# Kernel tuning notes

Hardware: AMD Instinct MI355X
Metric: run time of the kernel (lower is better)

## Reference

```python
import jax, jax.numpy as jnp
import numpy as np


def setup_inputs() -> dict:
    key = jax.random.key(0)
    ks = jax.random.split(key, 5)
    B, T, D, U, O = 128, 512, 512, 1024, 512
    x = jax.random.normal(ks[0], (B, T, D), dtype=jnp.float32)
    h0 = jnp.zeros((B, U), dtype=jnp.float32)
    c0 = jnp.zeros((B, U), dtype=jnp.float32)
    # Keras LSTMCell params: kernel [D,4U], recurrent_kernel [U,4U], bias [4U]; gate order i,f,g,o
    kernel = jax.random.normal(ks[1], (D, 4 * U), dtype=jnp.float32) * (1.0 / np.sqrt(D))
    rec_kernel = jax.random.normal(ks[2], (U, 4 * U), dtype=jnp.float32) * (1.0 / np.sqrt(U))
    bias = jnp.zeros((4 * U,), dtype=jnp.float32)
    Wd = jax.random.normal(ks[3], (U, O), dtype=jnp.float32) * (1.0 / np.sqrt(U))
    bd = jnp.zeros((O,), dtype=jnp.float32)
    return {"x": x, "h0": h0, "c0": c0, "kernel": kernel, "rec_kernel": rec_kernel,
            "bias": bias, "Wd": Wd, "bd": bd}


def _lstm_decode(x, h0, c0, kernel, rec_kernel, bias, Wd, bd):
    U = h0.shape[-1]
    # Precompute input contribution for all timesteps in one big GEMM: [B,T,4U]
    xz = jnp.einsum("btd,dg->btg", x, kernel) + bias

    def step(carry, xz_t):
        h, c = carry
        z = xz_t + h @ rec_kernel                     # [B,4U]
        i, f, g, o = jnp.split(z, 4, axis=-1)         # Keras gate order i,f,g,o
        i = jax.nn.sigmoid(i)
        f = jax.nn.sigmoid(f)
        o = jax.nn.sigmoid(o)
        c = f * c + i * jnp.tanh(g)
        h = o * jnp.tanh(c)
        return (h, c), h

    (_, _), hs = jax.lax.scan(step, (h0, c0), jnp.swapaxes(xz, 0, 1))  # hs: [T,B,U]
    hs = jnp.swapaxes(hs, 0, 1)                       # [B,T,U]
    # Per-step dense projection (output_layer of BasicDecoder)
    return jnp.einsum("btu,uo->bto", hs, Wd) + bd


def reference(x, h0, c0, kernel, rec_kernel, bias, Wd, bd):
    return _lstm_decode(x, h0, c0, kernel, rec_kernel, bias, Wd, bd)
```

## Files before the change

kernel.cpp:

```cpp
#include <hip/hip_runtime.h>
#include <hip/hip_bf16.h>

#define B_   128
#define T_   512
#define D_   512
#define U_   1024
#define O_   512
#define K_   1536
#define G4U_ 4096
#define NBLK 256
#define HPITCH 1032

typedef __attribute__((ext_vector_type(8))) short short8;
typedef __attribute__((ext_vector_type(4))) float f32x4;
typedef __attribute__((ext_vector_type(4))) int int4v;

__device__ __align__(16) unsigned short g_xbf[(size_t)B_ * T_ * D_];
__device__ __align__(16) unsigned short g_Wt[(size_t)G4U_ * K_];
__device__ __align__(16) unsigned short g_Wdt[(size_t)O_ * U_];
__device__ __align__(16) unsigned short g_hall[(size_t)(T_ + 1) * B_ * U_];
__device__ unsigned int g_flag[NBLK * 32];

__device__ __forceinline__ unsigned short f2b(float f) {
  unsigned u = __float_as_uint(f);
  u += 0x7fffu + ((u >> 16) & 1u);
  return (unsigned short)(u >> 16);
}

__global__ void prep_kernel(const float* __restrict__ x, const float* __restrict__ h0,
                            const float* __restrict__ kern, const float* __restrict__ rkern,
                            const float* __restrict__ Wd) {
  size_t tid = (size_t)blockIdx.x * blockDim.x + threadIdx.x;
  size_t np  = (size_t)gridDim.x * blockDim.x;
  if (tid < NBLK * 32) g_flag[tid] = 0u;

  const size_t nx8 = (size_t)B_ * T_ * D_ / 8;
  const float4* xv = (const float4*)x;
  for (size_t i = tid; i < nx8; i += np) {
    float4 v0 = xv[2 * i], v1 = xv[2 * i + 1];
    unsigned short tmp[8];
    tmp[0] = f2b(v0.x); tmp[1] = f2b(v0.y); tmp[2] = f2b(v0.z); tmp[3] = f2b(v0.w);
    tmp[4] = f2b(v1.x); tmp[5] = f2b(v1.y); tmp[6] = f2b(v1.z); tmp[7] = f2b(v1.w);
    *(int4*)&g_xbf[i * 8] = *(const int4*)tmp;
  }

  const size_t nw = (size_t)G4U_ * (K_ / 8);
  for (size_t i = tid; i < nw; i += np) {
    size_t cg = i / (K_ / 8);
    int kb = (int)(i % (K_ / 8)) * 8;
    int c = (int)(cg >> 6), g = (int)((cg >> 4) & 3), j = (int)(cg & 15);
    int n = g * 1024 + (c << 4) + j;
    unsigned short tmp[8];
#pragma unroll
    for (int q = 0; q < 8; ++q) {
      int k = kb + q;
      float v = (k < 512) ? kern[(size_t)k * G4U_ + n] : rkern[(size_t)(k - 512) * G4U_ + n];
      tmp[q] = f2b(v);
    }
    *(int4*)&g_Wt[cg * K_ + kb] = *(const int4*)tmp;
  }

  const size_t nd = (size_t)O_ * (U_ / 8);
  for (size_t i = tid; i < nd; i += np) {
    int o  = (int)(i >> 7);
    int ub = (int)(i & 127) * 8;
    unsigned short tmp[8];
#pragma unroll
    for (int q = 0; q < 8; ++q) tmp[q] = f2b(Wd[(size_t)(ub + q) * O_ + o]);
    *(int4*)&g_Wdt[(size_t)o * U_ + ub] = *(const int4*)tmp;
  }

  const size_t nh = (size_t)B_ * U_;
  for (size_t i = tid; i < nh; i += np) g_hall[i] = f2b(h0[i]);
}

__global__ __launch_bounds__(256, 1) void lstm_kernel(const float* __restrict__ c0,
                                                      const float* __restrict__ bias,
                                                      const float* __restrict__ bd,
                                                      float* __restrict__ out) {
  const int b    = blockIdx.x;
  const int tid  = threadIdx.x;
  const int wq   = tid >> 6;
  const int lane = tid & 63;
  const int rg   = lane >> 4;
  const int fr   = lane & 15;

  const int xcd = b & 7, idx = b >> 3;
  const int mg  = xcd >> 1;
  const int sl  = idx * 2 + (xcd & 1);
  const int lb  = mg * 64 + sl;
  const int m0  = mg * 32;
  const int ug  = sl;
  const int u0  = ug * 16;

  __shared__ __align__(16) unsigned short Ast[32 * HPITCH];
  __shared__ f32x4 zpo[4][32][17];
  __shared__ float po[4][16][20];

  short8 wzx[4][4], wzh[8][4];
#pragma unroll
  for (int kt = 0; kt < 4; ++kt)
#pragma unroll
    for (int g = 0; g < 4; ++g)
      wzx[kt][g] = *(const short8*)&g_Wt[(size_t)(ug * 64 + g * 16 + fr) * K_ +
                                         wq * 128 + kt * 32 + rg * 8];
#pragma unroll
  for (int kt = 0; kt < 8; ++kt)
#pragma unroll
    for (int g = 0; g < 4; ++g)
      wzh[kt][g] = *(const short8*)&g_Wt[(size_t)(ug * 64 + g * 16 + fr) * K_ +
                                         512 + wq * 256 + kt * 32 + rg * 8];

  const int oc0 = (ug >> 1) * 16;
  const int orh = (ug & 1) * 16;
  short8 wd[8];
#pragma unroll
  for (int kt = 0; kt < 8; ++kt)
    wd[kt] = *(const short8*)&g_Wdt[(size_t)(oc0 + fr) * U_ + wq * 256 + kt * 32 + rg * 8];

  const int erow = tid >> 3;
  const int euu  = (tid & 7) * 2;
  float cv[2];
  f32x4 bv[2];
#pragma unroll
  for (int j = 0; j < 2; ++j) {
    cv[j] = c0[(size_t)(m0 + erow) * U_ + u0 + euu + j];
    f32x4 tv;
#pragma unroll
    for (int g = 0; g < 4; ++g) tv[g] = bias[g * 1024 + u0 + euu + j];
    bv[j] = tv;
  }

  const int orow = tid >> 4, ocl = tid & 15;
  const float bd_v = bd[oc0 + ocl];

  const int xcol = wq * 128 + rg * 8;
  const unsigned short* ahp0 = &Ast[(size_t)fr * HPITCH + wq * 256 + rg * 8];
  const unsigned short* ahp1 = ahp0 + 16 * HPITCH;
  const unsigned short* aop  = &Ast[(size_t)(orh + fr) * HPITCH + wq * 256 + rg * 8];

  const int srow = lane >> 5;
  const int sseg = lane & 31;

  short8 axf0[4], axf1[4];
  {
    const unsigned short* x0 = &g_xbf[((size_t)(m0 + fr) * T_ + 0) * D_ + xcol];
    const unsigned short* x1 = &g_xbf[((size_t)(m0 + 16 + fr) * T_ + 0) * D_ + xcol];
#pragma unroll
    for (int kt = 0; kt < 4; ++kt) {
      axf0[kt] = *(const short8*)&x0[kt * 32];
      axf1[kt] = *(const short8*)&x1[kt * 32];
    }
  }

  for (int t = 0; t <= T_; ++t) {
    f32x4 acc[2][4];
    if (t < T_) {
#pragma unroll
      for (int rt = 0; rt < 2; ++rt)
#pragma unroll
        for (int g = 0; g < 4; ++g) acc[rt][g] = (f32x4){0.f, 0.f, 0.f, 0.f};
#pragma unroll
      for (int kt = 0; kt < 4; ++kt)
#pragma unroll
        for (int g = 0; g < 4; ++g) {
          acc[0][g] = __builtin_amdgcn_mfma_f32_16x16x32_bf16(axf0[kt], wzx[kt][g], acc[0][g], 0, 0, 0);
          acc[1][g] = __builtin_amdgcn_mfma_f32_16x16x32_bf16(axf1[kt], wzx[kt][g], acc[1][g], 0, 0, 0);
        }
    }

    if (t > 0) {
      if (lane < 16) {
        unsigned int* fp = &g_flag[(mg * 64 + wq * 16 + lane) * 32];
        while (__hip_atomic_load(fp, __ATOMIC_RELAXED, __HIP_MEMORY_SCOPE_AGENT) <
               (unsigned)t)
          __builtin_amdgcn_s_sleep(1);
      }
      asm volatile("" ::: "memory");
    }

    {
      const size_t hb = (size_t)t * (B_ * U_);
      int4v bh[16];
#pragma unroll
      for (int q = 0; q < 16; ++q)
        bh[q] = *(const int4v*)&g_hall[hb + (size_t)(m0 + q + srow * 16) * U_ +
                                      wq * 256 + sseg * 8];
#pragma unroll
      for (int q = 0; q < 16; ++q)
        *(int4v*)&Ast[(size_t)(q + srow * 16) * HPITCH + wq * 256 + sseg * 8] = bh[q];
    }

    if (t < T_) {
#pragma unroll
      for (int kt = 0; kt < 8; ++kt) {
        short8 a0 = *(const short8*)&ahp0[kt * 32];
        short8 a1 = *(const short8*)&ahp1[kt * 32];
#pragma unroll
        for (int g = 0; g < 4; ++g) {
          acc[0][g] = __builtin_amdgcn_mfma_f32_16x16x32_bf16(a0, wzh[kt][g], acc[0][g], 0, 0, 0);
          acc[1][g] = __builtin_amdgcn_mfma_f32_16x16x32_bf16(a1, wzh[kt][g], acc[1][g], 0, 0, 0);
        }
      }

#pragma unroll
      for (int rt = 0; rt < 2; ++rt)
#pragma unroll
        for (int r = 0; r < 4; ++r) {
          f32x4 v = {acc[rt][0][r], acc[rt][1][r], acc[rt][2][r], acc[rt][3][r]};
          zpo[wq][rt * 16 + rg * 4 + r][fr] = v;
        }
      __syncthreads();

      {
        unsigned short* hn = &g_hall[(size_t)(t + 1) * (B_ * U_)];
        float hv[2];
#pragma unroll
        for (int j = 0; j < 2; ++j) {
          f32x4 z = zpo[0][erow][euu + j] + zpo[1][erow][euu + j] +
                    zpo[2][erow][euu + j] + zpo[3][erow][euu + j];
          z += bv[j];
          float ig = 1.f / (1.f + __expf(-z[0]));
          float fg = 1.f / (1.f + __expf(-z[1]));
          float gg = tanhf(z[2]);
          float og = 1.f / (1.f + __expf(-z[3]));
          cv[j] = fg * cv[j] + ig * gg;
          hv[j] = og * tanhf(cv[j]);
        }
        unsigned int pk = (unsigned)f2b(hv[0]) | ((unsigned)f2b(hv[1]) << 16);
        *(volatile unsigned int*)&hn[(size_t)(m0 + erow) * U_ + u0 + euu] = pk;
      }
      __syncthreads();

      if (tid == 0)
        __hip_atomic_store(&g_flag[lb * 32], (unsigned)(t + 1), __ATOMIC_RELAXED,
                           __HIP_MEMORY_SCOPE_AGENT);

      if (t + 1 < T_) {
        const unsigned short* x0 = &g_xbf[((size_t)(m0 + fr) * T_ + (t + 1)) * D_ + xcol];
        const unsigned short* x1 = &g_xbf[((size_t)(m0 + 16 + fr) * T_ + (t + 1)) * D_ + xcol];
#pragma unroll
        for (int kt = 0; kt < 4; ++kt) {
          axf0[kt] = *(const short8*)&x0[kt * 32];
          axf1[kt] = *(const short8*)&x1[kt * 32];
        }
      }
    }

    if (t > 0) {
      f32x4 oa = {0.f, 0.f, 0.f, 0.f};
#pragma unroll
      for (int kt = 0; kt < 8; ++kt)
        oa = __builtin_amdgcn_mfma_f32_16x16x32_bf16(*(const short8*)&aop[kt * 32],
                                                     wd[kt], oa, 0, 0, 0);
#pragma unroll
      for (int r = 0; r < 4; ++r) po[wq][rg * 4 + r][fr] = oa[r];
      __syncthreads();
      float v = po[0][orow][ocl] + po[1][orow][ocl] + po[2][orow][ocl] +
                po[3][orow][ocl] + bd_v;
      out[((size_t)(m0 + orh + orow) * T_ + (t - 1)) * O_ + oc0 + ocl] = v;
    }
  }
}

extern "C" void kernel_launch(void* const* d_in, const int* in_sizes, int n_in,
                              void* d_out, int out_size, void* d_ws, size_t ws_size,
                              hipStream_t stream) {
  const float* x    = (const float*)d_in[0];
  const float* h0   = (const float*)d_in[1];
  const float* c0   = (const float*)d_in[2];
  const float* kern = (const float*)d_in[3];
  const float* rk   = (const float*)d_in[4];
  const float* bias = (const float*)d_in[5];
  const float* Wd   = (const float*)d_in[6];
  const float* bd   = (const float*)d_in[7];
  float* out = (float*)d_out;
  (void)in_sizes; (void)n_in; (void)d_ws; (void)ws_size; (void)out_size;

  prep_kernel<<<dim3(1024), dim3(256), 0, stream>>>(x, h0, kern, rk, Wd);
  lstm_kernel<<<dim3(NBLK), dim3(256), 0, stream>>>(c0, bias, bd, out);
}
```

Baseline: 2.621 ms.

## Use per-wave completion flags and split h-load to overlap with recurrent MFMA

Each wave now publishes its own completion flag after draining its stores, replacing the block-wide barrier plus single-thread flag store. Consumers wait on the flags for the first half of the hidden columns, load that half, and start the first half of the recurrent MFMAs while the second half's flags and loads complete. The gate activations switch to a fast reciprocal-based sigmoid and a tanh built from exp. This shortens the critical path of the cross-block step synchronisation, at the cost of more flag polling and a slightly less accurate tanh.

```diff
diff --git a/kernel.cpp b/kernel.cpp
--- a/kernel.cpp
+++ b/kernel.cpp
@@ -25,6 +25,13 @@
   unsigned u = __float_as_uint(f);
   u += 0x7fffu + ((u >> 16) & 1u);
   return (unsigned short)(u >> 16);
+}
+
+__device__ __forceinline__ float sigm_f(float x) {
+  return __builtin_amdgcn_rcpf(1.f + __expf(-x));
+}
+__device__ __forceinline__ float tanh_f(float x) {
+  return 1.f - 2.f * __builtin_amdgcn_rcpf(1.f + __expf(2.f * x));
 }
 
 __global__ void prep_kernel(const float* __restrict__ x, const float* __restrict__ h0,
@@ -139,8 +146,8 @@
   const unsigned short* ahp1 = ahp0 + 16 * HPITCH;
   const unsigned short* aop  = &Ast[(size_t)(orh + fr) * HPITCH + wq * 256 + rg * 8];
 
-  const int srow = lane >> 5;
-  const int sseg = lane & 31;
+  const int srow4 = lane >> 4;
+  const int sseg  = lane & 15;
 
   short8 axf0[4], axf1[4];
   {
@@ -169,31 +176,58 @@
         }
     }
 
+    const size_t hb = (size_t)t * (B_ * U_);
+    int4v bhA[8], bhB[8];
+
     if (t > 0) {
-      if (lane < 16) {
-        unsigned int* fp = &g_flag[(mg * 64 + wq * 16 + lane) * 32];
+      if (lane < 32) {
+        unsigned int* fp = &g_flag[(mg * 64 + wq * 16 + (lane >> 2)) * 32 + (lane & 3) * 8];
         while (__hip_atomic_load(fp, __ATOMIC_RELAXED, __HIP_MEMORY_SCOPE_AGENT) <
                (unsigned)t)
           __builtin_amdgcn_s_sleep(1);
       }
       asm volatile("" ::: "memory");
     }
-
-    {
-      const size_t hb = (size_t)t * (B_ * U_);
-      int4v bh[16];
-#pragma unroll
-      for (int q = 0; q < 16; ++q)
-        bh[q] = *(const int4v*)&g_hall[hb + (size_t)(m0 + q + srow * 16) * U_ +
-                                      wq * 256 + sseg * 8];
-#pragma unroll
-      for (int q = 0; q < 16; ++q)
-        *(int4v*)&Ast[(size_t)(q + srow * 16) * HPITCH + wq * 256 + sseg * 8] = bh[q];
-    }
-
+#pragma unroll
+    for (int q = 0; q < 8; ++q)
+      bhA[q] = *(const int4v*)&g_hall[hb + (size_t)(m0 + 4 * q + srow4) * U_ +
+                                     wq * 256 + sseg * 8];
+
+    if (t > 0) {
+      if (lane < 32) {
+        unsigned int* fp = &g_flag[(mg * 64 + wq * 16 + 8 + (lane >> 2)) * 32 + (lane & 3) * 8];
+        while (__hip_atomic_load(fp, __ATOMIC_RELAXED, __HIP_MEMORY_SCOPE_AGENT) <
+               (unsigned)t)
+          __builtin_amdgcn_s_sleep(1);
+      }
+      asm volatile("" ::: "memory");
+    }
+#pragma unroll
+    for (int q = 0; q < 8; ++q)
+      bhB[q] = *(const int4v*)&g_hall[hb + (size_t)(m0 + 4 * q + srow4) * U_ +
+                                     wq * 256 + 128 + sseg * 8];
+
+#pragma unroll
+    for (int q = 0; q < 8; ++q)
+      *(int4v*)&Ast[(size_t)(4 * q + srow4) * HPITCH + wq * 256 + sseg * 8] = bhA[q];
     if (t < T_) {
 #pragma unroll
-      for (int kt = 0; kt < 8; ++kt) {
+      for (int kt = 0; kt < 4; ++kt) {
+        short8 a0 = *(const short8*)&ahp0[kt * 32];
+        short8 a1 = *(const short8*)&ahp1[kt * 32];
+#pragma unroll
+        for (int g = 0; g < 4; ++g) {
+          acc[0][g] = __builtin_amdgcn_mfma_f32_16x16x32_bf16(a0, wzh[kt][g], acc[0][g], 0, 0, 0);
+          acc[1][g] = __builtin_amdgcn_mfma_f32_16x16x32_bf16(a1, wzh[kt][g], acc[1][g], 0, 0, 0);
+        }
+      }
+    }
+#pragma unroll
+    for (int q = 0; q < 8; ++q)
+      *(int4v*)&Ast[(size_t)(4 * q + srow4) * HPITCH + wq * 256 + 128 + sseg * 8] = bhB[q];
+    if (t < T_) {
+#pragma unroll
+      for (int kt = 4; kt < 8; ++kt) {
         short8 a0 = *(const short8*)&ahp0[kt * 32];
         short8 a1 = *(const short8*)&ahp1[kt * 32];
 #pragma unroll
@@ -220,21 +254,21 @@
           f32x4 z = zpo[0][erow][euu + j] + zpo[1][erow][euu + j] +
                     zpo[2][erow][euu + j] + zpo[3][erow][euu + j];
           z += bv[j];
-          float ig = 1.f / (1.f + __expf(-z[0]));
-          float fg = 1.f / (1.f + __expf(-z[1]));
-          float gg = tanhf(z[2]);
-          float og = 1.f / (1.f + __expf(-z[3]));
+          float ig = sigm_f(z[0]);
+          float fg = sigm_f(z[1]);
+          float gg = tanh_f(z[2]);
+          float og = sigm_f(z[3]);
           cv[j] = fg * cv[j] + ig * gg;
-          hv[j] = og * tanhf(cv[j]);
+          hv[j] = og * tanh_f(cv[j]);
         }
         unsigned int pk = (unsigned)f2b(hv[0]) | ((unsigned)f2b(hv[1]) << 16);
         *(volatile unsigned int*)&hn[(size_t)(m0 + erow) * U_ + u0 + euu] = pk;
       }
-      __syncthreads();
-
-      if (tid == 0)
-        __hip_atomic_store(&g_flag[lb * 32], (unsigned)(t + 1), __ATOMIC_RELAXED,
-                           __HIP_MEMORY_SCOPE_AGENT);
+
+      asm volatile("s_waitcnt vmcnt(0)" ::: "memory");
+      if (lane == 0)
+        __hip_atomic_store(&g_flag[lb * 32 + wq * 8], (unsigned)(t + 1),
+                           __ATOMIC_RELAXED, __HIP_MEMORY_SCOPE_AGENT);
 
       if (t + 1 < T_) {
         const unsigned short* x0 = &g_xbf[((size_t)(m0 + fr) * T_ + (t + 1)) * D_ + xcol];
@@ -245,6 +279,7 @@
           axf1[kt] = *(const short8*)&x1[kt * 32];
         }
       }
+      if (t == 0) __syncthreads();
     }
 
     if (t > 0) {
```

Result: slower. 2.772 ms (+5.8%).

## Replace per-block flag barrier with sentinel-polled hidden-state data

Applied to the files above, without the earlier changes.

Drops the global flag array and the post-step __syncthreads plus flag store. Instead, prep fills all future hidden-state slots with a NaN sentinel, and consumers poll the h data directly, reloading only the chunks still holding the sentinel. This removes one barrier and one flag round trip from each recurrent step. It also swaps tanhf and division for rcp/exp-based sigmoid and tanh. Risks include relying on the sentinel never matching a real bf16 pair, memory-ordering assumptions about the stores, and the extra work of filling the whole history buffer.

```diff
diff --git a/kernel.cpp b/kernel.cpp
--- a/kernel.cpp
+++ b/kernel.cpp
@@ -10,6 +10,7 @@
 #define G4U_ 4096
 #define NBLK 256
 #define HPITCH 1032
+#define SENT  ((int)0x7FC07FC0)
 
 typedef __attribute__((ext_vector_type(8))) short short8;
 typedef __attribute__((ext_vector_type(4))) float f32x4;
@@ -19,12 +20,18 @@
 __device__ __align__(16) unsigned short g_Wt[(size_t)G4U_ * K_];
 __device__ __align__(16) unsigned short g_Wdt[(size_t)O_ * U_];
 __device__ __align__(16) unsigned short g_hall[(size_t)(T_ + 1) * B_ * U_];
-__device__ unsigned int g_flag[NBLK * 32];
 
 __device__ __forceinline__ unsigned short f2b(float f) {
   unsigned u = __float_as_uint(f);
   u += 0x7fffu + ((u >> 16) & 1u);
   return (unsigned short)(u >> 16);
+}
+
+__device__ __forceinline__ float sigm_f(float x) {
+  return __builtin_amdgcn_rcpf(1.f + __expf(-x));
+}
+__device__ __forceinline__ float tanh_f(float x) {
+  return 1.f - 2.f * __builtin_amdgcn_rcpf(1.f + __expf(2.f * x));
 }
 
 __global__ void prep_kernel(const float* __restrict__ x, const float* __restrict__ h0,
@@ -32,7 +39,6 @@
                             const float* __restrict__ Wd) {
   size_t tid = (size_t)blockIdx.x * blockDim.x + threadIdx.x;
   size_t np  = (size_t)gridDim.x * blockDim.x;
-  if (tid < NBLK * 32) g_flag[tid] = 0u;
 
   const size_t nx8 = (size_t)B_ * T_ * D_ / 8;
   const float4* xv = (const float4*)x;
@@ -72,6 +78,13 @@
 
   const size_t nh = (size_t)B_ * U_;
   for (size_t i = tid; i < nh; i += np) g_hall[i] = f2b(h0[i]);
+
+  {
+    int4v sv; sv[0] = SENT; sv[1] = SENT; sv[2] = SENT; sv[3] = SENT;
+    int4v* hs = (int4v*)&g_hall[(size_t)B_ * U_];
+    const size_t ns4 = (size_t)T_ * B_ * U_ / 8;
+    for (size_t i = tid; i < ns4; i += np) hs[i] = sv;
+  }
 }
 
 __global__ __launch_bounds__(256, 1) void lstm_kernel(const float* __restrict__ c0,
@@ -88,7 +101,6 @@
   const int xcd = b & 7, idx = b >> 3;
   const int mg  = xcd >> 1;
   const int sl  = idx * 2 + (xcd & 1);
-  const int lb  = mg * 64 + sl;
   const int m0  = mg * 32;
   const int ug  = sl;
   const int u0  = ug * 16;
@@ -169,23 +181,28 @@
         }
     }
 
-    if (t > 0) {
-      if (lane < 16) {
-        unsigned int* fp = &g_flag[(mg * 64 + wq * 16 + lane) * 32];
-        while (__hip_atomic_load(fp, __ATOMIC_RELAXED, __HIP_MEMORY_SCOPE_AGENT) <
-               (unsigned)t)
-          __builtin_amdgcn_s_sleep(1);
-      }
-      asm volatile("" ::: "memory");
-    }
-
     {
       const size_t hb = (size_t)t * (B_ * U_);
       int4v bh[16];
-#pragma unroll
-      for (int q = 0; q < 16; ++q)
-        bh[q] = *(const int4v*)&g_hall[hb + (size_t)(m0 + q + srow * 16) * U_ +
-                                      wq * 256 + sseg * 8];
+      unsigned pend = 0xFFFFu;
+      while (true) {
+#pragma unroll
+        for (int q = 0; q < 16; ++q)
+          if (pend & (1u << q))
+            bh[q] = *(volatile const int4v*)&g_hall[hb + (size_t)(m0 + q + srow * 16) * U_ +
+                                                   wq * 256 + sseg * 8];
+        unsigned np = 0u;
+#pragma unroll
+        for (int q = 0; q < 16; ++q)
+          if (pend & (1u << q)) {
+            int4v v = bh[q];
+            if (v[0] == SENT || v[1] == SENT || v[2] == SENT || v[3] == SENT)
+              np |= (1u << q);
+          }
+        pend = np;
+        if (!pend) break;
+        __builtin_amdgcn_s_sleep(1);
+      }
 #pragma unroll
       for (int q = 0; q < 16; ++q)
         *(int4v*)&Ast[(size_t)(q + srow * 16) * HPITCH + wq * 256 + sseg * 8] = bh[q];
@@ -220,21 +237,16 @@
           f32x4 z = zpo[0][erow][euu + j] + zpo[1][erow][euu + j] +
                     zpo[2][erow][euu + j] + zpo[3][erow][euu + j];
           z += bv[j];
-          float ig = 1.f / (1.f + __expf(-z[0]));
-          float fg = 1.f / (1.f + __expf(-z[1]));
-          float gg = tanhf(z[2]);
-          float og = 1.f / (1.f + __expf(-z[3]));
+          float ig = sigm_f(z[0]);
+          float fg = sigm_f(z[1]);
+          float gg = tanh_f(z[2]);
+          float og = sigm_f(z[3]);
           cv[j] = fg * cv[j] + ig * gg;
-          hv[j] = og * tanhf(cv[j]);
+          hv[j] = og * tanh_f(cv[j]);
         }
         unsigned int pk = (unsigned)f2b(hv[0]) | ((unsigned)f2b(hv[1]) << 16);
         *(volatile unsigned int*)&hn[(size_t)(m0 + erow) * U_ + u0 + euu] = pk;
       }
-      __syncthreads();
-
-      if (tid == 0)
-        __hip_atomic_store(&g_flag[lb * 32], (unsigned)(t + 1), __ATOMIC_RELAXED,
-                           __HIP_MEMORY_SCOPE_AGENT);
 
       if (t + 1 < T_) {
         const unsigned short* x0 = &g_xbf[((size_t)(m0 + fr) * T_ + (t + 1)) * D_ + xcol];
@@ -245,6 +257,7 @@
           axf1[kt] = *(const short8*)&x1[kt * 32];
         }
       }
+      if (t == 0) __syncthreads();
     }
 
     if (t > 0) {
```

After: 5.014 ms. 1.91x slower.
